# Performance work log

Measured on AMD Instinct MI355X. Metric: run time of the kernel, lower is better.

## Reference

```python
import jax, jax.numpy as jnp
import numpy as np

N, L, D_MODEL, NUM_HEADS, MAX_SEQ = 4, 1024, 1024, 16, 2048
DEPTH = D_MODEL // NUM_HEADS


def setup_inputs() -> dict:
    key = jax.random.key(0)
    ks = jax.random.split(key, 12)
    inv = 1.0 / np.sqrt(D_MODEL)
    inp = {
        "q_in": jax.random.normal(ks[0], (N, L, D_MODEL), jnp.float32),
        "k_in": jax.random.normal(ks[1], (N, L, D_MODEL), jnp.float32),
        "v_in": jax.random.normal(ks[2], (N, L, D_MODEL), jnp.float32),
        # causal additive mask: 1.0 where attention is disallowed (j > i)
        "mask": (jnp.triu(jnp.ones((L, L), jnp.float32), k=1))[None, None, :, :],
        "Wq": jax.random.normal(ks[3], (D_MODEL, D_MODEL), jnp.float32) * inv,
        "bq": jnp.zeros((D_MODEL,), jnp.float32),
        "Wk": jax.random.normal(ks[4], (D_MODEL, D_MODEL), jnp.float32) * inv,
        "bk": jnp.zeros((D_MODEL,), jnp.float32),
        "Wv": jax.random.normal(ks[5], (D_MODEL, D_MODEL), jnp.float32) * inv,
        "bv": jnp.zeros((D_MODEL,), jnp.float32),
        "Wo": jax.random.normal(ks[6], (D_MODEL, D_MODEL), jnp.float32) * inv,
        "bo": jnp.zeros((D_MODEL,), jnp.float32),
        "pos_emb": jax.random.normal(ks[7], (MAX_SEQ, DEPTH), jnp.float32) * 0.02,
    }
    return inp


def _rel_bias(q, pos_emb):
    """q: [N,H,L,depth] -> skewed relative-position bias s: [N,H,L,L]."""
    n, h, l, d = q.shape
    e = pos_emb[pos_emb.shape[0] - l:, :]                     # [L, depth]
    qe = jnp.einsum('nhld,md->nhlm', q, e)                    # [N,H,L,L]
    # keep only the last (i+1) entries of row i (upper-left triangle zeroed)
    m = qe.shape[-1]
    keep = (jnp.arange(m)[None, :] >= (m - 1 - jnp.arange(l))[:, None]).astype(qe.dtype)
    qe = qe * keep
    # skew via pad/reshape/slice
    padded = jnp.pad(qe, ((0, 0), (0, 0), (0, 0), (1, 0)))    # [N,H,L,L+1]
    s = padded.reshape(n, h, l + 1, l)[:, :, 1:, :]           # [N,H,L,L]
    return s


def reference(q_in, k_in, v_in, mask, Wq, bq, Wk, bk, Wv, bv, Wo, bo, pos_emb):
    n, l, dm = q_in.shape
    h, d = NUM_HEADS, DEPTH

    def split(x):
        return x.reshape(n, l, h, d).transpose(0, 2, 1, 3)    # [N,H,L,depth]

    q = split(q_in @ Wq + bq)
    k = split(k_in @ Wk + bk)
    v = split(v_in @ Wv + bv)

    s = _rel_bias(q, pos_emb)
    logits = (jnp.einsum('nhld,nhmd->nhlm', q, k) + s) / jnp.sqrt(jnp.float32(d))
    logits = logits + mask * (-1e9)
    attn = jax.nn.softmax(logits, axis=-1)                    # [N,H,L,L]
    out = jnp.einsum('nhlm,nhmd->nhld', attn, v)
    out = out.transpose(0, 2, 1, 3).reshape(n, l, dm)
    return out @ Wo + bo
```

## Files before the change

### kernel.cpp

```cpp
#include <hip/hip_runtime.h>

typedef unsigned short u16t;
typedef unsigned int   u32t;
typedef __bf16 bf16x8 __attribute__((ext_vector_type(8)));
typedef float  f32x4  __attribute__((ext_vector_type(4)));

#define NB     4
#define SEQ    1024
#define DMODEL 1024
#define NHEAD  16
#define DEPTH  64
#define MAXSEQ 2048
#define MTOK   (NB * SEQ)

#define AS1 __attribute__((address_space(1)))
#define AS3 __attribute__((address_space(3)))

__device__ __forceinline__ u16t f2bf(float f) {
  return __builtin_bit_cast(u16t, (__bf16)f);
}
__device__ __forceinline__ float bf2f(u16t h) {
  return __builtin_bit_cast(float, (u32t)h << 16);
}
__device__ __forceinline__ void load_lds16(const void* g, void* l) {
  __builtin_amdgcn_global_load_lds((AS1 u32t*)(g), (AS3 u32t*)(l), 16, 0, 0);
}

__global__ void cvt3_kernel(const float* __restrict__ a, const float* __restrict__ b,
                            const float* __restrict__ c,
                            u16t* __restrict__ oa, u16t* __restrict__ ob,
                            u16t* __restrict__ oc, int n8) {
  int i = blockIdx.x * blockDim.x + threadIdx.x;
  if (i >= n8) return;
  const float* src = (blockIdx.z == 0) ? a : ((blockIdx.z == 1) ? b : c);
  u16t* dst = (blockIdx.z == 0) ? oa : ((blockIdx.z == 1) ? ob : oc);
  const float4* s4 = (const float4*)src;
  float4 x = s4[2 * i], y = s4[2 * i + 1];
  u16t tmp[8] = { f2bf(x.x), f2bf(x.y), f2bf(x.z), f2bf(x.w),
                  f2bf(y.x), f2bf(y.y), f2bf(y.z), f2bf(y.w) };
  ((uint4*)dst)[i] = *(const uint4*)tmp;
}

__global__ void transpose4_kernel(const float* __restrict__ w0, const float* __restrict__ w1,
                                  const float* __restrict__ w2, const float* __restrict__ w3,
                                  u16t* __restrict__ t0, u16t* __restrict__ t1,
                                  u16t* __restrict__ t2, u16t* __restrict__ t3,
                                  const float* __restrict__ pe, u16t* __restrict__ Er) {
  const int z = blockIdx.z;
  if (z == 4) {
    const int flat = blockIdx.y * 32 + blockIdx.x;
    if (flat < 256) {
      const int idx = flat * 256 + threadIdx.x;
      const int r = idx >> 6, d = idx & 63;
      Er[idx] = f2bf(pe[(size_t)(MAXSEQ - 1 - r) * DEPTH + d]);
    }
    return;
  }
  const float* W = (z == 0) ? w0 : ((z == 1) ? w1 : ((z == 2) ? w2 : w3));
  u16t* WT = (z == 0) ? t0 : ((z == 1) ? t1 : ((z == 2) ? t2 : t3));
  __shared__ float tile[32][33];
  const int tx = threadIdx.x & 31, ty = threadIdx.x >> 5;
  const int bx = blockIdx.x * 32, by = blockIdx.y * 32;
#pragma unroll
  for (int r = 0; r < 32; r += 8)
    tile[ty + r][tx] = W[(size_t)(by + ty + r) * DMODEL + bx + tx];
  __syncthreads();
#pragma unroll
  for (int r = 0; r < 32; r += 8)
    WT[(size_t)(bx + ty + r) * DMODEL + by + tx] = f2bf(tile[tx][ty + r]);
}

__device__ __forceinline__ void xcd_remap(int& bx, int& by) {
  const int flat = blockIdx.x + 8 * blockIdx.y;
  const int xv = flat & 7, pos = flat >> 3;
  bx = pos & 7;
  by = xv * 4 + (pos >> 3);
}

template <typename OutT>
__device__ __forceinline__ void gemm_bt_body(
    const u16t* __restrict__ A, const u16t* __restrict__ BT,
    const float* __restrict__ bias, OutT* __restrict__ C,
    int M, int Nc, int K, int bx, int by, float scale) {
  __shared__ __align__(16) u16t As[128 * 32];
  __shared__ __align__(16) u16t Bs[128 * 32];
  const int tid = threadIdx.x;
  const int wave = tid >> 6;
  const int lane = tid & 63;
  const int q = lane >> 4, t = lane & 15;
  const int lrow = lane >> 2, lch = lane & 3;
  const int bm = by * 128, bn = bx * 128;
  const int wi = (wave >> 1) * 64, wj = (wave & 1) * 64;

  f32x4 acc[4][4];
#pragma unroll
  for (int i = 0; i < 4; ++i)
#pragma unroll
    for (int j = 0; j < 4; ++j) acc[i][j] = f32x4{0.f, 0.f, 0.f, 0.f};

  for (int kt = 0; kt < K; kt += 32) {
    __syncthreads();
#pragma unroll
    for (int it = 0; it < 2; ++it) {
      const int rb = it * 64 + wave * 16;
      const u16t* ga = A + (size_t)(bm + rb + lrow) * K + kt + lch * 8;
      const u16t* gb = BT + (size_t)(bn + rb + lrow) * K + kt + lch * 8;
      load_lds16(ga, As + rb * 32);
      load_lds16(gb, Bs + rb * 32);
    }
    __syncthreads();
    bf16x8 af[4], bfr[4];
#pragma unroll
    for (int i = 0; i < 4; ++i) {
      af[i]  = *(const bf16x8*)(As + (wi + i * 16 + t) * 32 + q * 8);
      bfr[i] = *(const bf16x8*)(Bs + (wj + i * 16 + t) * 32 + q * 8);
    }
#pragma unroll
    for (int i = 0; i < 4; ++i)
#pragma unroll
      for (int j = 0; j < 4; ++j)
        acc[i][j] = __builtin_amdgcn_mfma_f32_16x16x32_bf16(af[i], bfr[j], acc[i][j], 0, 0, 0);
  }
#pragma unroll
  for (int j = 0; j < 4; ++j) {
    const int col = bn + wj + j * 16 + t;
    const float bv = bias[col];
#pragma unroll
    for (int i = 0; i < 4; ++i) {
#pragma unroll
      for (int r = 0; r < 4; ++r) {
        const int row = bm + wi + i * 16 + q * 4 + r;
        float v = (acc[i][j][r] + bv) * scale;
        if constexpr (sizeof(OutT) == 2) {
          C[(size_t)row * Nc + col] = f2bf(v);
        } else {
          C[(size_t)row * Nc + col] = v;
        }
      }
    }
  }
}

__global__ __launch_bounds__(256, 3) void gemm_qkv_kernel(
    const u16t* qa, const u16t* ka, const u16t* va,
    const u16t* wq, const u16t* wk, const u16t* wv,
    const float* bq, const float* bk, const float* bv,
    u16t* qo, u16t* ko, u16t* vo) {
  const int z = blockIdx.z;
  const u16t* A = (z == 0) ? qa : ((z == 1) ? ka : va);
  const u16t* B = (z == 0) ? wq : ((z == 1) ? wk : wv);
  const float* bb = (z == 0) ? bq : ((z == 1) ? bk : bv);
  u16t* C = (z == 0) ? qo : ((z == 1) ? ko : vo);
  const float scale = (z == 0) ? 0.125f : 1.0f;
  int bx, by;
  xcd_remap(bx, by);
  gemm_bt_body<u16t>(A, B, bb, C, MTOK, DMODEL, DMODEL, bx, by, scale);
}

__global__ __launch_bounds__(512) void gemm_out_kernel(
    const u16t* __restrict__ A, const u16t* __restrict__ W,
    const float* __restrict__ bias, float* __restrict__ C) {
  __shared__ __align__(16) u16t As[128 * 32];
  __shared__ __align__(16) u16t Bs[128 * 32];
  const int tid = threadIdx.x;
  const int wave = tid >> 6, lane = tid & 63;
  const int q = lane >> 4, t = lane & 15;
  const int srow = wave * 16 + (lane >> 2);
  const int sch = (lane & 3) * 8;
  int bx, by;
  xcd_remap(bx, by);
  const int bm = by * 128, bn = bx * 128;
  const int wi = (wave >> 1) * 32, wj = (wave & 1) * 64;
  const int K = DMODEL, Nc = DMODEL;

  f32x4 acc[2][4];
#pragma unroll
  for (int i = 0; i < 2; ++i)
#pragma unroll
    for (int j = 0; j < 4; ++j) acc[i][j] = f32x4{0.f, 0.f, 0.f, 0.f};

  for (int kt = 0; kt < K; kt += 32) {
    __syncthreads();
    load_lds16(A + (size_t)(bm + srow) * K + kt + sch, As + wave * 16 * 32);
    load_lds16(W + (size_t)(bn + srow) * K + kt + sch, Bs + wave * 16 * 32);
    __syncthreads();
    bf16x8 af[2], bfr[4];
#pragma unroll
    for (int i = 0; i < 2; ++i)
      af[i] = *(const bf16x8*)(As + (wi + i * 16 + t) * 32 + q * 8);
#pragma unroll
    for (int j = 0; j < 4; ++j)
      bfr[j] = *(const bf16x8*)(Bs + (wj + j * 16 + t) * 32 + q * 8);
#pragma unroll
    for (int i = 0; i < 2; ++i)
#pragma unroll
      for (int j = 0; j < 4; ++j)
        acc[i][j] = __builtin_amdgcn_mfma_f32_16x16x32_bf16(af[i], bfr[j], acc[i][j], 0, 0, 0);
  }
#pragma unroll
  for (int j = 0; j < 4; ++j) {
    const int col = bn + wj + j * 16 + t;
    const float bv = bias[col];
#pragma unroll
    for (int i = 0; i < 2; ++i) {
#pragma unroll
      for (int r = 0; r < 4; ++r) {
        const int row = bm + wi + i * 16 + q * 4 + r;
        C[(size_t)row * Nc + col] = acc[i][j][r] + bv;
      }
    }
  }
}

__global__ __launch_bounds__(512, 4) void attn_kernel(
    const u16t* __restrict__ Qp, const u16t* __restrict__ Kp,
    const u16t* __restrict__ Vp, const u16t* __restrict__ Er,
    u16t* __restrict__ AO) {
  const int gx = blockIdx.x;
  const int xcd = gx & 7, slot = gx >> 3;
  const int ghi = slot & 7, k4 = slot >> 3;
  const int T = (k4 < 4) ? (7 - k4) : (k4 - 4);
  const int g = (ghi << 3) | xcd;
  const int n = g >> 4, h = g & 15;

  const int tid = threadIdx.x;
  const int wave = tid >> 6, lane = tid & 63;
  const int q = lane >> 4, t = lane & 15;
  const int rr = tid >> 3;
  const int c0 = (tid & 7) * 8;

  __shared__ __align__(16) u16t Es[256 * 72];
  __shared__ __align__(16) u16t Ks[64 * 72];
  __shared__ __align__(16) u16t Vt[64 * 72];
  __shared__ __align__(16) u16t TP[8 * 1152];
  u16t* TPw = TP + wave * 1152;

  const int I0 = T * 128;
  const int iw = I0 + wave * 16;
  const int jmax = 2 * T + 1;

  const size_t qoff = ((size_t)(n * SEQ + iw + t)) * DMODEL + h * DEPTH;
  const bf16x8 qf0 = *(const bf16x8*)(Qp + qoff + q * 8);
  const bf16x8 qf1 = *(const bf16x8*)(Qp + qoff + 32 + q * 8);

  const uint4 epre0 = *(const uint4*)(Er + ((size_t)(2 * T) * 64 + rr) * DEPTH + c0);
  const uint4 epre1 = *(const uint4*)(Er + ((size_t)(2 * T + 1) * 64 + rr) * DEPTH + c0);
  const size_t kvoff0 = ((size_t)(n * SEQ + rr)) * DMODEL + h * DEPTH + c0;
  uint4 kv = *(const uint4*)(Kp + kvoff0);
  uint4 vv = *(const uint4*)(Vp + kvoff0);
  uint4 ev = *(const uint4*)(Er + ((ptrdiff_t)(2 * T - 1) * 64 + rr) * DEPTH + c0);

  *(uint4*)(Es + (((2 * T) & 3) * 64 + rr) * 72 + c0) = epre0;
  *(uint4*)(Es + (((2 * T + 1) & 3) * 64 + rr) * 72 + c0) = epre1;

  f32x4 o[4];
#pragma unroll
  for (int c = 0; c < 4; ++c) o[c] = f32x4{0.f, 0.f, 0.f, 0.f};
  float l_r[4] = {0.f, 0.f, 0.f, 0.f};

  for (int jt = 0; jt <= jmax; ++jt) {
    const int J0 = jt * 64;
    const int cnew = 2 * T - 1 - jt;

    __syncthreads();
    *(uint4*)(Ks + rr * 72 + c0) = kv;
    *(uint4*)(Es + ((cnew & 3) * 64 + rr) * 72 + c0) = ev;
    {
      const u16t* pv = (const u16t*)&vv;
#pragma unroll
      for (int uu = 0; uu < 8; ++uu) {
        const int d = c0 + uu;
        Vt[d * 72 + (rr ^ (((d >> 2) & 7) << 3))] = pv[uu];
      }
    }
    __syncthreads();

    if (jt < jmax) {
      const size_t kvoff = ((size_t)(n * SEQ + J0 + 64 + rr)) * DMODEL + h * DEPTH + c0;
      kv = *(const uint4*)(Kp + kvoff);
      vv = *(const uint4*)(Vp + kvoff);
      ev = *(const uint4*)(Er + ((ptrdiff_t)(cnew - 1) * 64 + rr) * DEPTH + c0);
    }

    __builtin_amdgcn_s_setprio(1);
    f32x4 s[4];
#pragma unroll
    for (int c = 0; c < 4; ++c) s[c] = f32x4{0.f, 0.f, 0.f, 0.f};
#pragma unroll
    for (int kk = 0; kk < 2; ++kk) {
      const bf16x8 qf = kk ? qf1 : qf0;
#pragma unroll
      for (int c = 0; c < 4; ++c) {
        const bf16x8 kf = *(const bf16x8*)(Ks + (c * 16 + t) * 72 + kk * 32 + q * 8);
        s[c] = __builtin_amdgcn_mfma_f32_16x16x32_bf16(qf, kf, s[c], 0, 0, 0);
      }
    }
    const int D0 = iw - J0 - 63;
    f32x4 tb[5];
#pragma unroll
    for (int cc = 0; cc < 5; ++cc) tb[cc] = f32x4{0.f, 0.f, 0.f, 0.f};
#pragma unroll
    for (int kk = 0; kk < 2; ++kk) {
      const bf16x8 qf = kk ? qf1 : qf0;
#pragma unroll
      for (int cc = 0; cc < 5; ++cc) {
        const int sl = (int)(((unsigned)(D0 + cc * 16 + t)) & 255u);
        const bf16x8 ef = *(const bf16x8*)(Es + sl * 72 + kk * 32 + q * 8);
        tb[cc] = __builtin_amdgcn_mfma_f32_16x16x32_bf16(qf, ef, tb[cc], 0, 0, 0);
      }
    }
    __builtin_amdgcn_s_setprio(0);
#pragma unroll
    for (int cc = 0; cc < 5; ++cc)
#pragma unroll
      for (int r = 0; r < 4; ++r) {
        const int kp = cc * 16 + t - q * 4 - r;
        if ((unsigned)kp < 64u)
          TPw[(q * 4 + r) * 72 + kp] = f2bf(tb[cc][r]);
      }

    const int dIJ = I0 - J0;
#pragma unroll
    for (int c = 0; c < 4; ++c) {
      const int jc = c * 16 + t;
#pragma unroll
      for (int r = 0; r < 4; ++r) {
        const int ic = wave * 16 + q * 4 + r;
        float lg = s[c][r] + bf2f(TPw[(q * 4 + r) * 72 + 63 - c * 16 - t]);
        lg = (jc <= ic + dIJ) ? lg : -1e30f;
        const float pr = __expf(lg);
        s[c][r] = pr;
        l_r[r] += pr;
      }
    }
#pragma unroll
    for (int c = 0; c < 4; ++c)
#pragma unroll
      for (int r = 0; r < 4; ++r)
        TPw[(q * 4 + r) * 72 + c * 16 + t] = f2bf(s[c][r]);

    const bf16x8 pf0 = *(const bf16x8*)(TPw + t * 72 + q * 8);
    const bf16x8 pf1 = *(const bf16x8*)(TPw + t * 72 + 32 + q * 8);
    __builtin_amdgcn_s_setprio(1);
#pragma unroll
    for (int c2 = 0; c2 < 4; ++c2) {
      const int dd = c2 * 16 + t;
      const int sw = (dd >> 2) & 7;
      const bf16x8 v0 = *(const bf16x8*)(Vt + dd * 72 + ((0 + q) ^ sw) * 8);
      const bf16x8 v1 = *(const bf16x8*)(Vt + dd * 72 + ((4 + q) ^ sw) * 8);
      o[c2] = __builtin_amdgcn_mfma_f32_16x16x32_bf16(pf0, v0, o[c2], 0, 0, 0);
      o[c2] = __builtin_amdgcn_mfma_f32_16x16x32_bf16(pf1, v1, o[c2], 0, 0, 0);
    }
    __builtin_amdgcn_s_setprio(0);
  }

#pragma unroll
  for (int r = 0; r < 4; ++r) {
    float lsum = l_r[r];
    lsum += __shfl_xor(lsum, 1, 64);
    lsum += __shfl_xor(lsum, 2, 64);
    lsum += __shfl_xor(lsum, 4, 64);
    lsum += __shfl_xor(lsum, 8, 64);
    const float inv = 1.f / lsum;
    const size_t obase = ((size_t)(n * SEQ + iw + q * 4 + r)) * DMODEL + h * DEPTH;
#pragma unroll
    for (int c2 = 0; c2 < 4; ++c2)
      AO[obase + c2 * 16 + t] = f2bf(o[c2][r] * inv);
  }
}

extern "C" void kernel_launch(void* const* d_in, const int* in_sizes, int n_in,
                              void* d_out, int out_size, void* d_ws, size_t ws_size,
                              hipStream_t stream) {
  const float* q_in = (const float*)d_in[0];
  const float* k_in = (const float*)d_in[1];
  const float* v_in = (const float*)d_in[2];
  const float* Wq = (const float*)d_in[4];
  const float* bq = (const float*)d_in[5];
  const float* Wk = (const float*)d_in[6];
  const float* bk = (const float*)d_in[7];
  const float* Wv = (const float*)d_in[8];
  const float* bv = (const float*)d_in[9];
  const float* Wo = (const float*)d_in[10];
  const float* bo = (const float*)d_in[11];
  const float* pe = (const float*)d_in[12];
  float* out = (float*)d_out;

  char* ws = (char*)d_ws;
  constexpr size_t MB = 1ull << 20;
  u16t* qb  = (u16t*)(ws);
  u16t* kb  = (u16t*)(ws + 8 * MB);
  u16t* vb  = (u16t*)(ws + 16 * MB);
  u16t* Qp  = (u16t*)(ws + 24 * MB);
  u16t* Kp  = (u16t*)(ws + 32 * MB);
  u16t* Vp  = (u16t*)(ws + 40 * MB);
  u16t* AOb = (u16t*)(ws + 48 * MB);
  u16t* WqT = (u16t*)(ws + 56 * MB);
  u16t* WkT = (u16t*)(ws + 58 * MB);
  u16t* WvT = (u16t*)(ws + 60 * MB);
  u16t* WoT = (u16t*)(ws + 62 * MB);
  u16t* Erl = (u16t*)(ws + 64 * MB + 16 * 1024);

  const size_t SZA = (size_t)MTOK * DMODEL;
  const int n8 = (int)(SZA / 8);
  cvt3_kernel<<<dim3(n8 / 256, 1, 3), 256, 0, stream>>>(q_in, k_in, v_in, qb, kb, vb, n8);
  transpose4_kernel<<<dim3(32, 32, 5), 256, 0, stream>>>(Wq, Wk, Wv, Wo, WqT, WkT, WvT, WoT,
                                                         pe, Erl);

  gemm_qkv_kernel<<<dim3(DMODEL / 128, MTOK / 128, 3), 256, 0, stream>>>(
      qb, kb, vb, WqT, WkT, WvT, bq, bk, bv, Qp, Kp, Vp);

  attn_kernel<<<dim3(512, 1, 1), 512, 0, stream>>>(Qp, Kp, Vp, Erl, AOb);

  gemm_out_kernel<<<dim3(DMODEL / 128, MTOK / 128, 1), 512, 0, stream>>>(AOb, WoT, bo, out);
}
```

Measured before the change: 238.8 us.

## Read rel-pos embeddings from global memory and double-buffer K/V tiles

Removes the 256-row LDS ring buffer for the relative-position embedding. Each wave now reads its E fragments directly from global memory (expected to hit in cache), with the row index clamped to the valid range. K and V get two LDS buffers, so the leading __syncthreads per iteration is dropped and only one barrier per tile remains. This frees a large share of LDS, which may allow more blocks per CU, but adds per-MFMA global load latency in the bias inner loop. Clamping rather than wrapping the index changes which rows are read for out-of-range positions, which relies on those entries being masked later.

```diff
diff --git a/kernel.cpp b/kernel.cpp
--- a/kernel.cpp
+++ b/kernel.cpp
@@ -229,9 +229,8 @@
   const int rr = tid >> 3;
   const int c0 = (tid & 7) * 8;
 
-  __shared__ __align__(16) u16t Es[256 * 72];
-  __shared__ __align__(16) u16t Ks[64 * 72];
-  __shared__ __align__(16) u16t Vt[64 * 72];
+  __shared__ __align__(16) u16t Ks[2][64 * 72];
+  __shared__ __align__(16) u16t Vt[2][64 * 72];
   __shared__ __align__(16) u16t TP[8 * 1152];
   u16t* TPw = TP + wave * 1152;
 
@@ -243,15 +242,9 @@
   const bf16x8 qf0 = *(const bf16x8*)(Qp + qoff + q * 8);
   const bf16x8 qf1 = *(const bf16x8*)(Qp + qoff + 32 + q * 8);
 
-  const uint4 epre0 = *(const uint4*)(Er + ((size_t)(2 * T) * 64 + rr) * DEPTH + c0);
-  const uint4 epre1 = *(const uint4*)(Er + ((size_t)(2 * T + 1) * 64 + rr) * DEPTH + c0);
   const size_t kvoff0 = ((size_t)(n * SEQ + rr)) * DMODEL + h * DEPTH + c0;
   uint4 kv = *(const uint4*)(Kp + kvoff0);
   uint4 vv = *(const uint4*)(Vp + kvoff0);
-  uint4 ev = *(const uint4*)(Er + ((ptrdiff_t)(2 * T - 1) * 64 + rr) * DEPTH + c0);
-
-  *(uint4*)(Es + (((2 * T) & 3) * 64 + rr) * 72 + c0) = epre0;
-  *(uint4*)(Es + (((2 * T + 1) & 3) * 64 + rr) * 72 + c0) = epre1;
 
   f32x4 o[4];
 #pragma unroll
@@ -260,17 +253,15 @@
 
   for (int jt = 0; jt <= jmax; ++jt) {
     const int J0 = jt * 64;
-    const int cnew = 2 * T - 1 - jt;
-
-    __syncthreads();
-    *(uint4*)(Ks + rr * 72 + c0) = kv;
-    *(uint4*)(Es + ((cnew & 3) * 64 + rr) * 72 + c0) = ev;
+    const int cur = jt & 1;
+
+    *(uint4*)(Ks[cur] + rr * 72 + c0) = kv;
     {
       const u16t* pv = (const u16t*)&vv;
 #pragma unroll
       for (int uu = 0; uu < 8; ++uu) {
         const int d = c0 + uu;
-        Vt[d * 72 + (rr ^ (((d >> 2) & 7) << 3))] = pv[uu];
+        Vt[cur][d * 72 + (rr ^ (((d >> 2) & 7) << 3))] = pv[uu];
       }
     }
     __syncthreads();
@@ -279,7 +270,6 @@
       const size_t kvoff = ((size_t)(n * SEQ + J0 + 64 + rr)) * DMODEL + h * DEPTH + c0;
       kv = *(const uint4*)(Kp + kvoff);
       vv = *(const uint4*)(Vp + kvoff);
-      ev = *(const uint4*)(Er + ((ptrdiff_t)(cnew - 1) * 64 + rr) * DEPTH + c0);
     }
 
     __builtin_amdgcn_s_setprio(1);
@@ -291,7 +281,7 @@
       const bf16x8 qf = kk ? qf1 : qf0;
 #pragma unroll
       for (int c = 0; c < 4; ++c) {
-        const bf16x8 kf = *(const bf16x8*)(Ks + (c * 16 + t) * 72 + kk * 32 + q * 8);
+        const bf16x8 kf = *(const bf16x8*)(Ks[cur] + (c * 16 + t) * 72 + kk * 32 + q * 8);
         s[c] = __builtin_amdgcn_mfma_f32_16x16x32_bf16(qf, kf, s[c], 0, 0, 0);
       }
     }
@@ -304,8 +294,9 @@
       const bf16x8 qf = kk ? qf1 : qf0;
 #pragma unroll
       for (int cc = 0; cc < 5; ++cc) {
-        const int sl = (int)(((unsigned)(D0 + cc * 16 + t)) & 255u);
-        const bf16x8 ef = *(const bf16x8*)(Es + sl * 72 + kk * 32 + q * 8);
+        int sl = D0 + cc * 16 + t;
+        sl = (sl < 0) ? 0 : ((sl > SEQ - 1) ? SEQ - 1 : sl);
+        const bf16x8 ef = *(const bf16x8*)(Er + (size_t)sl * DEPTH + kk * 32 + q * 8);
         tb[cc] = __builtin_amdgcn_mfma_f32_16x16x32_bf16(qf, ef, tb[cc], 0, 0, 0);
       }
     }
@@ -346,8 +337,8 @@
     for (int c2 = 0; c2 < 4; ++c2) {
       const int dd = c2 * 16 + t;
       const int sw = (dd >> 2) & 7;
-      const bf16x8 v0 = *(const bf16x8*)(Vt + dd * 72 + ((0 + q) ^ sw) * 8);
-      const bf16x8 v1 = *(const bf16x8*)(Vt + dd * 72 + ((4 + q) ^ sw) * 8);
+      const bf16x8 v0 = *(const bf16x8*)(Vt[cur] + dd * 72 + ((0 + q) ^ sw) * 8);
+      const bf16x8 v1 = *(const bf16x8*)(Vt[cur] + dd * 72 + ((4 + q) ^ sw) * 8);
       o[c2] = __builtin_amdgcn_mfma_f32_16x16x32_bf16(pf0, v0, o[c2], 0, 0, 0);
       o[c2] = __builtin_amdgcn_mfma_f32_16x16x32_bf16(pf1, v1, o[c2], 0, 0, 0);
     }
```

Result: slower. 271.2 us (+13.6%).
